# Performance work log

Measured on AMD Instinct MI355X. Metric: run time of the kernel, lower is better.

## Reference

```python
import jax, jax.numpy as jnp
import numpy as np

D_MODEL = 1024
N_HEADS = 16
D_K = D_MODEL // N_HEADS
D_FF = 4096
B, S = 4, 2048
EPS = 1e-5


def setup_inputs() -> dict:
    key = jax.random.key(0)
    ks = jax.random.split(key, 16)
    s = 0.02
    inp = {
        'x': jax.random.normal(ks[0], (B, S, D_MODEL), dtype=jnp.float32),
        'Wq': jax.random.normal(ks[1], (D_MODEL, D_MODEL), dtype=jnp.float32) * s,
        'bq': jnp.zeros((D_MODEL,), jnp.float32),
        'Wk': jax.random.normal(ks[2], (D_MODEL, D_MODEL), dtype=jnp.float32) * s,
        'bk': jnp.zeros((D_MODEL,), jnp.float32),
        'Wv': jax.random.normal(ks[3], (D_MODEL, D_MODEL), dtype=jnp.float32) * s,
        'bv': jnp.zeros((D_MODEL,), jnp.float32),
        'Wo': jax.random.normal(ks[4], (D_MODEL, D_MODEL), dtype=jnp.float32) * s,
        'bo': jnp.zeros((D_MODEL,), jnp.float32),
        'W1': jax.random.normal(ks[5], (D_MODEL, D_FF), dtype=jnp.float32) * s,
        'b1': jnp.zeros((D_FF,), jnp.float32),
        'W2': jax.random.normal(ks[6], (D_FF, D_MODEL), dtype=jnp.float32) * s,
        'b2': jnp.zeros((D_MODEL,), jnp.float32),
        'g1': jnp.ones((D_MODEL,), jnp.float32),
        'be1': jnp.zeros((D_MODEL,), jnp.float32),
        'g2': jnp.ones((D_MODEL,), jnp.float32),
        'be2': jnp.zeros((D_MODEL,), jnp.float32),
    }
    return inp


def _layernorm(x, g, b):
    mu = jnp.mean(x, axis=-1, keepdims=True)
    var = jnp.var(x, axis=-1, keepdims=True)
    return (x - mu) * jax.lax.rsqrt(var + EPS) * g + b


def reference(x, Wq, bq, Wk, bk, Wv, bv, Wo, bo, W1, b1, W2, b2, g1, be1, g2, be2):
    # Multi-head self-attention (mask=None, dropout in eval -> identity)
    q = (x @ Wq + bq).reshape(B, S, N_HEADS, D_K).transpose(0, 2, 1, 3)  # [B,H,S,Dk]
    k = (x @ Wk + bk).reshape(B, S, N_HEADS, D_K).transpose(0, 2, 1, 3)
    v = (x @ Wv + bv).reshape(B, S, N_HEADS, D_K).transpose(0, 2, 1, 3)
    scores = jnp.einsum('bhqd,bhkd->bhqk', q, k) / jnp.sqrt(jnp.float32(D_K))
    attn = jax.nn.softmax(scores, axis=-1)
    out = jnp.einsum('bhqk,bhkd->bhqd', attn, v)          # [B,H,S,Dk]
    out = out.transpose(0, 2, 1, 3).reshape(B, S, D_MODEL)
    att_out = out @ Wo + bo
    x2 = _layernorm(x + att_out, g1, be1)
    ff = jax.nn.relu(x2 @ W1 + b1) @ W2 + b2
    return _layernorm(x2 + ff, g2, be2)
```

## Files before the change

kernel.cpp:

```cpp
#include <hip/hip_runtime.h>
#include <hip/hip_bf16.h>

typedef __attribute__((ext_vector_type(8)))  __bf16 bf16x8;
typedef __attribute__((ext_vector_type(4)))  float  f32x4;
typedef __attribute__((ext_vector_type(16))) float  f32x16;

static __device__ __forceinline__ unsigned short f2bf(float x) {
    unsigned int u = __float_as_uint(x);
    unsigned int r = (u + 0x7FFFu + ((u >> 16) & 1u)) >> 16;
    return (unsigned short)r;
}
static __device__ __forceinline__ float bf2f(unsigned short u) {
    return __uint_as_float(((unsigned int)u) << 16);
}

static __device__ __forceinline__ float fast_exp2(float x) {
    float r;
    asm volatile("v_exp_f32 %0, %1\n\ts_nop 1" : "=v"(r) : "v"(x));
    return r;
}
static __device__ __forceinline__ unsigned int cvt_pk_bf16(float a, float b) {
    unsigned int r;
    asm("v_cvt_pk_bf16_f32 %0, %1, %2" : "=v"(r) : "v"(a), "v"(b));
    return r;
}

static __device__ __forceinline__ void gload_lds16(const ushort* g, ushort* l) {
    __builtin_amdgcn_global_load_lds((const __attribute__((address_space(1))) void*)g,
                                     (__attribute__((address_space(3))) void*)l, 16, 0, 0);
}

static __device__ __forceinline__ void barrier_fence() {
    __builtin_amdgcn_s_barrier();
    __builtin_amdgcn_sched_barrier(0);
    asm volatile("" ::: "memory");
}

static __device__ __forceinline__ int xcd_swz(int id, int nwg) {
    return (id & 7) * (nwg >> 3) + (id >> 3);
}

__global__ __launch_bounds__(256) void cast_bf16_kernel(const float* __restrict__ in,
                                                        ushort* __restrict__ out, int n4) {
    int i = blockIdx.x * 256 + threadIdx.x;
    if (i < n4) {
        float4 v = reinterpret_cast<const float4*>(in)[i];
        ushort4 o;
        o.x = f2bf(v.x); o.y = f2bf(v.y); o.z = f2bf(v.z); o.w = f2bf(v.w);
        reinterpret_cast<ushort4*>(out)[i] = o;
    }
}

__global__ __launch_bounds__(256) void transpose_cast_kernel(const float* __restrict__ in,
                                                             ushort* __restrict__ out,
                                                             int K, int N) {
    __shared__ float tile[32][33];
    const int tx = threadIdx.x;
    const int ty = threadIdx.y;
    const int n0 = blockIdx.x * 32;
    const int k0 = blockIdx.y * 32;
    for (int i = ty; i < 32; i += 8)
        tile[i][tx] = in[(size_t)(k0 + i) * N + n0 + tx];
    __syncthreads();
    for (int i = ty; i < 32; i += 8)
        out[(size_t)(n0 + i) * K + k0 + tx] = f2bf(tile[tx][i]);
}

__global__ __launch_bounds__(256) void transpose_cast3_kernel(const float* __restrict__ w0,
                                                              const float* __restrict__ w1,
                                                              const float* __restrict__ w2,
                                                              ushort* __restrict__ out) {
    __shared__ float tile[32][33];
    const int tx = threadIdx.x;
    const int ty = threadIdx.y;
    const int n0 = blockIdx.x * 32;
    const int k0 = blockIdx.y * 32;
    const int z  = blockIdx.z;
    const float* in = (z == 0) ? w0 : (z == 1 ? w1 : w2);
    ushort* o = out + (size_t)z * 1024 * 1024;
    for (int i = ty; i < 32; i += 8)
        tile[i][tx] = in[(size_t)(k0 + i) * 1024 + n0 + tx];
    __syncthreads();
    for (int i = ty; i < 32; i += 8)
        o[(size_t)(n0 + i) * 1024 + k0 + tx] = f2bf(tile[tx][i]);
}

template<int RELU, int OUTBF, int QKV>
__global__ __launch_bounds__(256) void gemm_p3(const ushort* __restrict__ A,
                                               const ushort* __restrict__ Bt,
                                               const float* __restrict__ b0,
                                               const float* __restrict__ b1_,
                                               const float* __restrict__ b2_,
                                               void* __restrict__ Cp,
                                               int M, int N, int K) {
    __shared__ ushort As[3][4096];
    __shared__ ushort Bs[3][4096];
    const int tid  = threadIdx.x;
    const int lane = tid & 63;
    const int w    = tid >> 6;
    const int wr   = w >> 1, wc = w & 1;
    const int nwg = gridDim.x * gridDim.y;
    int wid = xcd_swz(blockIdx.y * gridDim.x + blockIdx.x, nwg);
    const int bx = wid % gridDim.x;
    const int by = wid / gridDim.x;
    const int m0 = by * 128;
    const int n0 = bx * 128;
    const int lr = lane & 15;
    const int lk = (lane >> 4) * 8;

    const int r0 = w * 32 + (lane >> 2);
    const int c8 = (lane & 3) * 8;
    const ushort* gA0 = A  + (size_t)(m0 + r0)      * K + c8;
    const ushort* gA1 = A  + (size_t)(m0 + r0 + 16) * K + c8;
    const ushort* gB0 = Bt + (size_t)(n0 + r0)      * K + c8;
    const ushort* gB1 = Bt + (size_t)(n0 + r0 + 16) * K + c8;
    const int wb = w * 1024;

    f32x4 acc[4][4];
    const f32x4 z = {0.f, 0.f, 0.f, 0.f};
#pragma unroll
    for (int i = 0; i < 4; i++)
#pragma unroll
        for (int j = 0; j < 4; j++) acc[i][j] = z;

    const int nt = K >> 5;

#pragma unroll
    for (int t = 0; t < 2; ++t) {
        const int kn = t * 32;
        gload_lds16(gA0 + kn, &As[t][wb]);
        gload_lds16(gA1 + kn, &As[t][wb + 512]);
        gload_lds16(gB0 + kn, &Bs[t][wb]);
        gload_lds16(gB1 + kn, &Bs[t][wb + 512]);
    }

    int cur = 0;
    for (int t = 0; t < nt; ++t) {
        if (t + 1 < nt) asm volatile("s_waitcnt vmcnt(4)" ::: "memory");
        else            asm volatile("s_waitcnt vmcnt(0)" ::: "memory");
        barrier_fence();

        if (t + 2 < nt) {
            const int bi = (cur + 2 >= 3) ? cur - 1 : cur + 2;
            const int kn = (t + 2) * 32;
            gload_lds16(gA0 + kn, &As[bi][wb]);
            gload_lds16(gA1 + kn, &As[bi][wb + 512]);
            gload_lds16(gB0 + kn, &Bs[bi][wb]);
            gload_lds16(gB1 + kn, &Bs[bi][wb + 512]);
        }

        const ushort* Asb = As[cur];
        const ushort* Bsb = Bs[cur];
        bf16x8 af[4], bfr[4];
#pragma unroll
        for (int i = 0; i < 4; i++)
            af[i] = *reinterpret_cast<const bf16x8*>(&Asb[(wr * 64 + i * 16 + lr) * 32 + lk]);
#pragma unroll
        for (int j = 0; j < 4; j++)
            bfr[j] = *reinterpret_cast<const bf16x8*>(&Bsb[(wc * 64 + j * 16 + lr) * 32 + lk]);
#pragma unroll
        for (int i = 0; i < 4; i++)
#pragma unroll
            for (int j = 0; j < 4; j++)
                acc[i][j] = __builtin_amdgcn_mfma_f32_16x16x32_bf16(af[i], bfr[j], acc[i][j], 0, 0, 0);

        cur = (cur == 2) ? 0 : cur + 1;
    }

    const float* bias;
    float qscale = 1.0f;
    if (QKV) {
        bias = (n0 < 1024) ? b0 : (n0 < 2048 ? b1_ : b2_);
        if (n0 < 1024) qscale = 0.18033688f;
    } else {
        bias = b0;
    }
    const int nb = QKV ? (n0 & 1023) : n0;
    const int rbase = (lane >> 4) * 4;
#pragma unroll
    for (int i = 0; i < 4; i++) {
#pragma unroll
        for (int j = 0; j < 4; j++) {
            const int cloc = wc * 64 + j * 16 + lr;
            const float bv = bias[nb + cloc];
#pragma unroll
            for (int r = 0; r < 4; r++) {
                const int row = m0 + wr * 64 + i * 16 + rbase + r;
                float v = acc[i][j][r] + bv;
                if (RELU) v = v > 0.f ? v : 0.f;
                if (QKV)  v *= qscale;
                if (OUTBF) ((ushort*)Cp)[(size_t)row * N + n0 + cloc] = f2bf(v);
                else       ((float*)Cp)[(size_t)row * N + n0 + cloc] = v;
            }
        }
    }
}

#define ASWZ(row, col) ((row) * 64 + ((col) ^ ((((row) ^ ((row) >> 3)) & 7) << 3)))

__global__ __launch_bounds__(256, 3) void attn_kernel(const ushort* __restrict__ QKV,
                                                      ushort* __restrict__ O) {
    __shared__ ushort Ks[2][4096];
    __shared__ ushort Vt[2][4096];
    const int tid  = threadIdx.x;
    const int lane = tid & 63;
    const int w    = tid >> 6;
    const int l31  = lane & 31;
    const int hi   = lane >> 5;

    int blk = xcd_swz(blockIdx.x, gridDim.x);
    const int qb = blk & 15;
    const int h  = (blk >> 4) & 15;
    const int b  = blk >> 8;
    const int s0 = qb * 128 + w * 32;
    const size_t rowb   = (size_t)b * 2048;
    const size_t base_q = rowb * 3072 + (size_t)h * 64;
    const size_t base_k = base_q + 1024;
    const size_t base_v = base_q + 2048;
    const size_t base_o = rowb * 1024 + (size_t)h * 64;

    bf16x8 qf[4];
#pragma unroll
    for (int ks = 0; ks < 4; ks++)
        qf[ks] = *reinterpret_cast<const bf16x8*>(
            &QKV[base_q + (size_t)(s0 + l31) * 3072 + ks * 16 + 8 * hi]);

    int off8[2][4];
#pragma unroll
    for (int sub = 0; sub < 2; sub++)
#pragma unroll
        for (int ks = 0; ks < 4; ks++)
            off8[sub][ks] = ASWZ(sub * 32 + l31, ks * 16 + 8 * hi);

    const int tS  = tid >> 3;
    const int ccS = tid & 7;
    int vwoff[2][8];
#pragma unroll
    for (int i = 0; i < 2; i++)
#pragma unroll
        for (int jj = 0; jj < 8; jj++)
            vwoff[i][jj] = ASWZ(ccS * 8 + jj, tS + i * 32);
    const int t1  = tS + 32;
    const int sz0 = (tS ^ (tS >> 3)) & 7;
    const int sz1 = (t1 ^ (t1 >> 3)) & 7;
    const ushort* pK0 = QKV + base_k + (size_t)tS * 3072 + (ccS ^ sz0) * 8;
    const ushort* pK1 = QKV + base_k + (size_t)t1 * 3072 + (ccS ^ sz1) * 8;
    const ushort* pV0 = QKV + base_v + (size_t)tS * 3072 + ccS * 8;
    const ushort* pV1 = QKV + base_v + (size_t)t1 * 3072 + ccS * 8;
    const size_t step = (size_t)64 * 3072;

    gload_lds16(pK0, &Ks[0][w * 512]);
    gload_lds16(pK1, &Ks[0][2048 + w * 512]);
    {
        int4 v0 = *reinterpret_cast<const int4*>(pV0);
        int4 v1 = *reinterpret_cast<const int4*>(pV1);
        const ushort* vs0 = reinterpret_cast<const ushort*>(&v0);
        const ushort* vs1 = reinterpret_cast<const ushort*>(&v1);
#pragma unroll
        for (int jj = 0; jj < 8; jj++) Vt[0][vwoff[0][jj]] = vs0[jj];
#pragma unroll
        for (int jj = 0; jj < 8; jj++) Vt[0][vwoff[1][jj]] = vs1[jj];
    }
    pK0 += step; pK1 += step; pV0 += step; pV1 += step;
    __syncthreads();

    f32x16 oacc0, oacc1;
    for (int i = 0; i < 16; i++) { oacc0[i] = 0.f; oacc1[i] = 0.f; }
    float lacc = 0.f;
    int cur = 0;

    for (int it = 0; it < 32; ++it) {
        int4 nv0, nv1;
        if (it < 31) {
            gload_lds16(pK0, &Ks[cur ^ 1][w * 512]);
            gload_lds16(pK1, &Ks[cur ^ 1][2048 + w * 512]);
            nv0 = *reinterpret_cast<const int4*>(pV0);
            nv1 = *reinterpret_cast<const int4*>(pV1);
            pK0 += step; pK1 += step; pV0 += step; pV1 += step;
        }

        f32x16 sa0, sa1;
        for (int i = 0; i < 16; i++) { sa0[i] = 0.f; sa1[i] = 0.f; }
        __builtin_amdgcn_s_setprio(1);
#pragma unroll
        for (int ks = 0; ks < 4; ks++) {
            bf16x8 k0 = *reinterpret_cast<const bf16x8*>(&Ks[cur][off8[0][ks]]);
            sa0 = __builtin_amdgcn_mfma_f32_32x32x16_bf16(k0, qf[ks], sa0, 0, 0, 0);
        }
#pragma unroll
        for (int ks = 0; ks < 4; ks++) {
            bf16x8 k1 = *reinterpret_cast<const bf16x8*>(&Ks[cur][off8[1][ks]]);
            sa1 = __builtin_amdgcn_mfma_f32_32x32x16_bf16(k1, qf[ks], sa1, 0, 0, 0);
        }
        __builtin_amdgcn_s_setprio(0);

        unsigned pk0[8], pk1[8];
#pragma unroll
        for (int i = 0; i < 8; i++) {
            float plo = fast_exp2(sa0[2 * i]);
            float phi = fast_exp2(sa0[2 * i + 1]);
            lacc += plo + phi;
            pk0[i] = cvt_pk_bf16(plo, phi);
        }
#pragma unroll
        for (int i = 0; i < 8; i++) {
            float plo = fast_exp2(sa1[2 * i]);
            float phi = fast_exp2(sa1[2 * i + 1]);
            lacc += plo + phi;
            pk1[i] = cvt_pk_bf16(plo, phi);
        }

        __builtin_amdgcn_s_setprio(1);
#pragma unroll
        for (int ks = 0; ks < 4; ks++) {
            const int bi = 4 * (ks & 1);
            unsigned a, bb, c, d;
            if (ks < 2) { a = pk0[bi]; bb = pk0[bi + 1]; c = pk0[bi + 2]; d = pk0[bi + 3]; }
            else        { a = pk1[bi]; bb = pk1[bi + 1]; c = pk1[bi + 2]; d = pk1[bi + 3]; }
            asm("v_permlane32_swap_b32 %0, %1" : "+v"(a), "+v"(c));
            asm("v_permlane32_swap_b32 %0, %1" : "+v"(bb), "+v"(d));
            union { unsigned u[4]; bf16x8 v; } fr;
            fr.u[0] = a; fr.u[1] = bb; fr.u[2] = c; fr.u[3] = d;
            bf16x8 v0 = *reinterpret_cast<const bf16x8*>(&Vt[cur][off8[0][ks]]);
            oacc0 = __builtin_amdgcn_mfma_f32_32x32x16_bf16(fr.v, v0, oacc0, 0, 0, 0);
            bf16x8 v1 = *reinterpret_cast<const bf16x8*>(&Vt[cur][off8[1][ks]]);
            oacc1 = __builtin_amdgcn_mfma_f32_32x32x16_bf16(fr.v, v1, oacc1, 0, 0, 0);
        }
        __builtin_amdgcn_s_setprio(0);

        if (it < 31) {
            const ushort* vs0 = reinterpret_cast<const ushort*>(&nv0);
            const ushort* vs1 = reinterpret_cast<const ushort*>(&nv1);
#pragma unroll
            for (int jj = 0; jj < 8; jj++) Vt[cur ^ 1][vwoff[0][jj]] = vs0[jj];
#pragma unroll
            for (int jj = 0; jj < 8; jj++) Vt[cur ^ 1][vwoff[1][jj]] = vs1[jj];
        }
        __syncthreads();
        cur ^= 1;
    }

    const float ltot = lacc + __shfl_xor(lacc, 32);
    const float inv  = 1.f / ltot;
#pragma unroll
    for (int r = 0; r < 16; r++) {
        const int qloc = (r & 3) + 8 * (r >> 2) + 4 * hi;
        const float invq = __shfl(inv, qloc);
        const size_t rowoff = base_o + (size_t)(s0 + qloc) * 1024 + l31;
        O[rowoff]      = f2bf(oacc0[r] * invq);
        O[rowoff + 32] = f2bf(oacc1[r] * invq);
    }
}

__global__ __launch_bounds__(256) void ln_res_fb(const float* __restrict__ x,
                                                 const ushort* __restrict__ y,
                                                 const float* __restrict__ g,
                                                 const float* __restrict__ be,
                                                 ushort* __restrict__ outb) {
    const int row = blockIdx.x;
    const int tid = threadIdx.x;
    const float4 xv = reinterpret_cast<const float4*>(x + (size_t)row * 1024)[tid];
    const ushort4 yv = reinterpret_cast<const ushort4*>(y + (size_t)row * 1024)[tid];
    float v[4] = {xv.x + bf2f(yv.x), xv.y + bf2f(yv.y), xv.z + bf2f(yv.z), xv.w + bf2f(yv.w)};
    float s  = v[0] + v[1] + v[2] + v[3];
    float s2 = v[0]*v[0] + v[1]*v[1] + v[2]*v[2] + v[3]*v[3];
    for (int off = 32; off; off >>= 1) { s += __shfl_down(s, off); s2 += __shfl_down(s2, off); }
    __shared__ float red[8];
    const int w = tid >> 6, lane = tid & 63;
    if (lane == 0) { red[w] = s; red[4 + w] = s2; }
    __syncthreads();
    if (tid == 0) {
        const float ts  = red[0] + red[1] + red[2] + red[3];
        const float ts2 = red[4] + red[5] + red[6] + red[7];
        const float mu  = ts * (1.f / 1024.f);
        const float var = ts2 * (1.f / 1024.f) - mu * mu;
        red[0] = mu;
        red[1] = rsqrtf(var + 1e-5f);
    }
    __syncthreads();
    const float mu = red[0], rs = red[1];
    const float4 gv = reinterpret_cast<const float4*>(g)[tid];
    const float4 bv = reinterpret_cast<const float4*>(be)[tid];
    ushort4 ob;
    ob.x = f2bf((v[0] - mu) * rs * gv.x + bv.x);
    ob.y = f2bf((v[1] - mu) * rs * gv.y + bv.y);
    ob.z = f2bf((v[2] - mu) * rs * gv.z + bv.z);
    ob.w = f2bf((v[3] - mu) * rs * gv.w + bv.w);
    reinterpret_cast<ushort4*>(outb + (size_t)row * 1024)[tid] = ob;
}

__global__ __launch_bounds__(256) void ln_res_bb(const ushort* __restrict__ x,
                                                 const ushort* __restrict__ y,
                                                 const float* __restrict__ g,
                                                 const float* __restrict__ be,
                                                 float* __restrict__ outf) {
    const int row = blockIdx.x;
    const int tid = threadIdx.x;
    const ushort4 xv = reinterpret_cast<const ushort4*>(x + (size_t)row * 1024)[tid];
    const ushort4 yv = reinterpret_cast<const ushort4*>(y + (size_t)row * 1024)[tid];
    float v[4] = {bf2f(xv.x) + bf2f(yv.x), bf2f(xv.y) + bf2f(yv.y),
                  bf2f(xv.z) + bf2f(yv.z), bf2f(xv.w) + bf2f(yv.w)};
    float s  = v[0] + v[1] + v[2] + v[3];
    float s2 = v[0]*v[0] + v[1]*v[1] + v[2]*v[2] + v[3]*v[3];
    for (int off = 32; off; off >>= 1) { s += __shfl_down(s, off); s2 += __shfl_down(s2, off); }
    __shared__ float red[8];
    const int w = tid >> 6, lane = tid & 63;
    if (lane == 0) { red[w] = s; red[4 + w] = s2; }
    __syncthreads();
    if (tid == 0) {
        const float ts  = red[0] + red[1] + red[2] + red[3];
        const float ts2 = red[4] + red[5] + red[6] + red[7];
        const float mu  = ts * (1.f / 1024.f);
        const float var = ts2 * (1.f / 1024.f) - mu * mu;
        red[0] = mu;
        red[1] = rsqrtf(var + 1e-5f);
    }
    __syncthreads();
    const float mu = red[0], rs = red[1];
    const float4 gv = reinterpret_cast<const float4*>(g)[tid];
    const float4 bv = reinterpret_cast<const float4*>(be)[tid];
    float4 of;
    of.x = (v[0] - mu) * rs * gv.x + bv.x;
    of.y = (v[1] - mu) * rs * gv.y + bv.y;
    of.z = (v[2] - mu) * rs * gv.z + bv.z;
    of.w = (v[3] - mu) * rs * gv.w + bv.w;
    reinterpret_cast<float4*>(outf + (size_t)row * 1024)[tid] = of;
}

extern "C" void kernel_launch(void* const* d_in, const int* in_sizes, int n_in,
                              void* d_out, int out_size, void* d_ws, size_t ws_size,
                              hipStream_t stream) {
    const float* x  = (const float*)d_in[0];
    const float* Wq = (const float*)d_in[1];  const float* bq = (const float*)d_in[2];
    const float* Wk = (const float*)d_in[3];  const float* bk = (const float*)d_in[4];
    const float* Wv = (const float*)d_in[5];  const float* bv = (const float*)d_in[6];
    const float* Wo = (const float*)d_in[7];  const float* bo = (const float*)d_in[8];
    const float* W1 = (const float*)d_in[9];  const float* b1 = (const float*)d_in[10];
    const float* W2 = (const float*)d_in[11]; const float* b2 = (const float*)d_in[12];
    const float* g1 = (const float*)d_in[13]; const float* be1 = (const float*)d_in[14];
    const float* g2 = (const float*)d_in[15]; const float* be2 = (const float*)d_in[16];

    char* ws = (char*)d_ws;
    const size_t MBy = (size_t)1 << 20;
    ushort* xb    = (ushort*)(ws + 0 * MBy);
    ushort* wqkvT = (ushort*)(ws + 16 * MBy);
    ushort* woT   = (ushort*)(ws + 22 * MBy);
    ushort* w1T   = (ushort*)(ws + 24 * MBy);
    ushort* w2T   = (ushort*)(ws + 32 * MBy);
    ushort* QKVb  = (ushort*)(ws + 40 * MBy);
    ushort* AOb   = (ushort*)(ws + 88 * MBy);
    ushort* h1    = (ushort*)(ws + 40 * MBy);
    ushort* y1b   = (ushort*)(ws + 104 * MBy);
    ushort* y2b   = (ushort*)(ws + 104 * MBy);
    ushort* x2b   = (ushort*)(ws + 120 * MBy);
    (void)ws_size; (void)n_in; (void)in_sizes; (void)out_size;

    const int M = 8192;

    cast_bf16_kernel<<<(M * 1024 / 4 + 255) / 256, 256, 0, stream>>>(x, xb, M * 1024 / 4);
    dim3 tb(32, 8);
    transpose_cast3_kernel<<<dim3(32, 32, 3), tb, 0, stream>>>(Wq, Wk, Wv, wqkvT);
    transpose_cast_kernel<<<dim3(32, 32),  tb, 0, stream>>>(Wo, woT, 1024, 1024);
    transpose_cast_kernel<<<dim3(128, 32), tb, 0, stream>>>(W1, w1T, 1024, 4096);
    transpose_cast_kernel<<<dim3(32, 128), tb, 0, stream>>>(W2, w2T, 4096, 1024);

    gemm_p3<0, 1, 1><<<dim3(24, 64), 256, 0, stream>>>(xb, wqkvT, bq, bk, bv, QKVb,
                                                       M, 3072, 1024);

    attn_kernel<<<1024, 256, 0, stream>>>(QKVb, AOb);

    gemm_p3<0, 1, 0><<<dim3(8, 64), 256, 0, stream>>>(AOb, woT, bo, nullptr, nullptr, y1b,
                                                      M, 1024, 1024);

    ln_res_fb<<<M, 256, 0, stream>>>(x, y1b, g1, be1, x2b);

    gemm_p3<1, 1, 0><<<dim3(32, 64), 256, 0, stream>>>(x2b, w1T, b1, nullptr, nullptr, h1,
                                                       M, 4096, 1024);
    gemm_p3<0, 1, 0><<<dim3(8, 64), 256, 0, stream>>>(h1, w2T, b2, nullptr, nullptr, y2b,
                                                      M, 1024, 4096);

    ln_res_bb<<<M, 256, 0, stream>>>(x2b, y2b, g2, be2, (float*)d_out);
}
```

Baseline: 428.7 us.

## Enlarge GEMM tiles to 256x128 with 8 waves, BK=64 and swizzled LDS

Replaces the 128x128, 4-wave GEMM with a 256x128 tile computed by 8 waves. The K step doubles to 64 and the LDS layout uses an XOR swizzle to avoid bank conflicts on the fragment reads, and MFMA blocks are wrapped in s_setprio. The aim is better operand reuse per byte loaded, fewer barriers per unit of K, and fewer LDS conflicts. The cost is much higher LDS use (~144KB across 3 stages), which may limit occupancy, plus fewer workgroups for the N=1024 GEMMs.

```diff
diff --git a/kernel.cpp b/kernel.cpp
--- a/kernel.cpp
+++ b/kernel.cpp
@@ -86,35 +86,62 @@
 }
 
 template<int RELU, int OUTBF, int QKV>
-__global__ __launch_bounds__(256) void gemm_p3(const ushort* __restrict__ A,
-                                               const ushort* __restrict__ Bt,
-                                               const float* __restrict__ b0,
-                                               const float* __restrict__ b1_,
-                                               const float* __restrict__ b2_,
-                                               void* __restrict__ Cp,
-                                               int M, int N, int K) {
-    __shared__ ushort As[3][4096];
-    __shared__ ushort Bs[3][4096];
+__global__ __launch_bounds__(512, 2) void gemm_8p(const ushort* __restrict__ A,
+                                                  const ushort* __restrict__ Bt,
+                                                  const float* __restrict__ b0,
+                                                  const float* __restrict__ b1_,
+                                                  const float* __restrict__ b2_,
+                                                  void* __restrict__ Cp,
+                                                  int M, int N, int K) {
+    __shared__ ushort As[3][16384];
+    __shared__ ushort Bs[3][8192];
     const int tid  = threadIdx.x;
     const int lane = tid & 63;
     const int w    = tid >> 6;
-    const int wr   = w >> 1, wc = w & 1;
-    const int nwg = gridDim.x * gridDim.y;
+    const int wr   = w >> 1;
+    const int wc   = w & 1;
+    const int nwg  = gridDim.x * gridDim.y;
     int wid = xcd_swz(blockIdx.y * gridDim.x + blockIdx.x, nwg);
     const int bx = wid % gridDim.x;
     const int by = wid / gridDim.x;
-    const int m0 = by * 128;
+    const int m0 = by * 256;
     const int n0 = bx * 128;
     const int lr = lane & 15;
-    const int lk = (lane >> 4) * 8;
-
-    const int r0 = w * 32 + (lane >> 2);
-    const int c8 = (lane & 3) * 8;
-    const ushort* gA0 = A  + (size_t)(m0 + r0)      * K + c8;
-    const ushort* gA1 = A  + (size_t)(m0 + r0 + 16) * K + c8;
-    const ushort* gB0 = Bt + (size_t)(n0 + r0)      * K + c8;
-    const ushort* gB1 = Bt + (size_t)(n0 + r0 + 16) * K + c8;
-    const int wb = w * 1024;
+    const int lg = lane >> 4;
+
+    int offA[4][2], offB[4][2];
+#pragma unroll
+    for (int i = 0; i < 4; i++) {
+        const int row = wr * 64 + i * 16 + lr;
+#pragma unroll
+        for (int ks = 0; ks < 2; ks++)
+            offA[i][ks] = row * 64 + (((ks * 4 + lg) ^ (row & 7)) << 3);
+    }
+#pragma unroll
+    for (int j = 0; j < 4; j++) {
+        const int row = wc * 64 + j * 16 + lr;
+#pragma unroll
+        for (int ks = 0; ks < 2; ks++)
+            offB[j][ks] = row * 64 + (((ks * 4 + lg) ^ (row & 7)) << 3);
+    }
+
+    const int cp = lane & 7;
+    const ushort* gA[4];
+    int ldsA[4];
+#pragma unroll
+    for (int a = 0; a < 4; a++) {
+        const int row = a * 64 + w * 8 + (lane >> 3);
+        gA[a]  = A + (size_t)(m0 + row) * K + ((cp ^ (row & 7)) << 3);
+        ldsA[a] = (a * 512 + w * 64) * 8;
+    }
+    const ushort* gB[2];
+    int ldsB[2];
+#pragma unroll
+    for (int b = 0; b < 2; b++) {
+        const int row = b * 64 + w * 8 + (lane >> 3);
+        gB[b]  = Bt + (size_t)(n0 + row) * K + ((cp ^ (row & 7)) << 3);
+        ldsB[b] = (b * 512 + w * 64) * 8;
+    }
 
     f32x4 acc[4][4];
     const f32x4 z = {0.f, 0.f, 0.f, 0.f};
@@ -123,46 +150,67 @@
 #pragma unroll
         for (int j = 0; j < 4; j++) acc[i][j] = z;
 
-    const int nt = K >> 5;
+    const int nt = K >> 6;
 
 #pragma unroll
     for (int t = 0; t < 2; ++t) {
-        const int kn = t * 32;
-        gload_lds16(gA0 + kn, &As[t][wb]);
-        gload_lds16(gA1 + kn, &As[t][wb + 512]);
-        gload_lds16(gB0 + kn, &Bs[t][wb]);
-        gload_lds16(gB1 + kn, &Bs[t][wb + 512]);
+        const int kn = t * 64;
+#pragma unroll
+        for (int a = 0; a < 4; a++) gload_lds16(gA[a] + kn, &As[t][ldsA[a]]);
+#pragma unroll
+        for (int b = 0; b < 2; b++) gload_lds16(gB[b] + kn, &Bs[t][ldsB[b]]);
     }
 
     int cur = 0;
     for (int t = 0; t < nt; ++t) {
-        if (t + 1 < nt) asm volatile("s_waitcnt vmcnt(4)" ::: "memory");
+        if (t + 1 < nt) asm volatile("s_waitcnt vmcnt(6)" ::: "memory");
         else            asm volatile("s_waitcnt vmcnt(0)" ::: "memory");
         barrier_fence();
 
         if (t + 2 < nt) {
-            const int bi = (cur + 2 >= 3) ? cur - 1 : cur + 2;
-            const int kn = (t + 2) * 32;
-            gload_lds16(gA0 + kn, &As[bi][wb]);
-            gload_lds16(gA1 + kn, &As[bi][wb + 512]);
-            gload_lds16(gB0 + kn, &Bs[bi][wb]);
-            gload_lds16(gB1 + kn, &Bs[bi][wb + 512]);
+            const int bi = (cur + 2 > 2) ? cur - 1 : cur + 2;
+            const int kn = (t + 2) * 64;
+#pragma unroll
+            for (int a = 0; a < 4; a++) gload_lds16(gA[a] + kn, &As[bi][ldsA[a]]);
+#pragma unroll
+            for (int b = 0; b < 2; b++) gload_lds16(gB[b] + kn, &Bs[bi][ldsB[b]]);
         }
 
         const ushort* Asb = As[cur];
         const ushort* Bsb = Bs[cur];
-        bf16x8 af[4], bfr[4];
-#pragma unroll
-        for (int i = 0; i < 4; i++)
-            af[i] = *reinterpret_cast<const bf16x8*>(&Asb[(wr * 64 + i * 16 + lr) * 32 + lk]);
-#pragma unroll
-        for (int j = 0; j < 4; j++)
-            bfr[j] = *reinterpret_cast<const bf16x8*>(&Bsb[(wc * 64 + j * 16 + lr) * 32 + lk]);
-#pragma unroll
-        for (int i = 0; i < 4; i++)
+
+        {
+            bf16x8 af[4], bfr[4];
+#pragma unroll
+            for (int i = 0; i < 4; i++)
+                af[i] = *reinterpret_cast<const bf16x8*>(&Asb[offA[i][0]]);
 #pragma unroll
             for (int j = 0; j < 4; j++)
-                acc[i][j] = __builtin_amdgcn_mfma_f32_16x16x32_bf16(af[i], bfr[j], acc[i][j], 0, 0, 0);
+                bfr[j] = *reinterpret_cast<const bf16x8*>(&Bsb[offB[j][0]]);
+            __builtin_amdgcn_s_setprio(1);
+#pragma unroll
+            for (int i = 0; i < 4; i++)
+#pragma unroll
+                for (int j = 0; j < 4; j++)
+                    acc[i][j] = __builtin_amdgcn_mfma_f32_16x16x32_bf16(af[i], bfr[j], acc[i][j], 0, 0, 0);
+            __builtin_amdgcn_s_setprio(0);
+        }
+        {
+            bf16x8 af[4], bfr[4];
+#pragma unroll
+            for (int i = 0; i < 4; i++)
+                af[i] = *reinterpret_cast<const bf16x8*>(&Asb[offA[i][1]]);
+#pragma unroll
+            for (int j = 0; j < 4; j++)
+                bfr[j] = *reinterpret_cast<const bf16x8*>(&Bsb[offB[j][1]]);
+            __builtin_amdgcn_s_setprio(1);
+#pragma unroll
+            for (int i = 0; i < 4; i++)
+#pragma unroll
+                for (int j = 0; j < 4; j++)
+                    acc[i][j] = __builtin_amdgcn_mfma_f32_16x16x32_bf16(af[i], bfr[j], acc[i][j], 0, 0, 0);
+            __builtin_amdgcn_s_setprio(0);
+        }
 
         cur = (cur == 2) ? 0 : cur + 1;
     }
@@ -464,19 +512,19 @@
     transpose_cast_kernel<<<dim3(128, 32), tb, 0, stream>>>(W1, w1T, 1024, 4096);
     transpose_cast_kernel<<<dim3(32, 128), tb, 0, stream>>>(W2, w2T, 4096, 1024);
 
-    gemm_p3<0, 1, 1><<<dim3(24, 64), 256, 0, stream>>>(xb, wqkvT, bq, bk, bv, QKVb,
+    gemm_8p<0, 1, 1><<<dim3(24, 32), 512, 0, stream>>>(xb, wqkvT, bq, bk, bv, QKVb,
                                                        M, 3072, 1024);
 
     attn_kernel<<<1024, 256, 0, stream>>>(QKVb, AOb);
 
-    gemm_p3<0, 1, 0><<<dim3(8, 64), 256, 0, stream>>>(AOb, woT, bo, nullptr, nullptr, y1b,
+    gemm_8p<0, 1, 0><<<dim3(8, 32), 512, 0, stream>>>(AOb, woT, bo, nullptr, nullptr, y1b,
                                                       M, 1024, 1024);
 
     ln_res_fb<<<M, 256, 0, stream>>>(x, y1b, g1, be1, x2b);
 
-    gemm_p3<1, 1, 0><<<dim3(32, 64), 256, 0, stream>>>(x2b, w1T, b1, nullptr, nullptr, h1,
+    gemm_8p<1, 1, 0><<<dim3(32, 32), 512, 0, stream>>>(x2b, w1T, b1, nullptr, nullptr, h1,
                                                        M, 4096, 1024);
-    gemm_p3<0, 1, 0><<<dim3(8, 64), 256, 0, stream>>>(h1, w2T, b2, nullptr, nullptr, y2b,
+    gemm_8p<0, 1, 0><<<dim3(8, 32), 512, 0, stream>>>(h1, w2T, b2, nullptr, nullptr, y2b,
                                                       M, 1024, 4096);
 
     ln_res_bb<<<M, 256, 0, stream>>>(x2b, y2b, g2, be2, (float*)d_out);
```

Result: slower. 446.4 us (+4.1%).

## Fuse residual adds into GEMM epilogues and pack V-transpose LDS writes

Applied to the files above, without the earlier changes.

Moves the residual addition (x after the Wo projection, x2 after W2) into the GEMM epilogues, so the layernorm kernels read one bf16 tensor instead of two. The attention kernel now assigns each thread two adjacent V rows and writes pairs of bf16 values as 32-bit LDS stores, halving the scalar LDS writes during the V transpose. The exp asm loses its volatile qualifier and trailing s_nop so the compiler can schedule it. The residual is now rounded to bf16 together with the GEMM output before layernorm, which slightly changes precision.

```diff
diff --git a/kernel.cpp b/kernel.cpp
--- a/kernel.cpp
+++ b/kernel.cpp
@@ -16,7 +16,7 @@
 
 static __device__ __forceinline__ float fast_exp2(float x) {
     float r;
-    asm volatile("v_exp_f32 %0, %1\n\ts_nop 1" : "=v"(r) : "v"(x));
+    asm("v_exp_f32 %0, %1" : "=v"(r) : "v"(x));
     return r;
 }
 static __device__ __forceinline__ unsigned int cvt_pk_bf16(float a, float b) {
@@ -85,12 +85,13 @@
         o[(size_t)(n0 + i) * 1024 + k0 + tx] = f2bf(tile[tx][i]);
 }
 
-template<int RELU, int OUTBF, int QKV>
+template<int RELU, int OUTBF, int QKV, int RES>
 __global__ __launch_bounds__(256) void gemm_p3(const ushort* __restrict__ A,
                                                const ushort* __restrict__ Bt,
                                                const float* __restrict__ b0,
                                                const float* __restrict__ b1_,
                                                const float* __restrict__ b2_,
+                                               const void* __restrict__ xres,
                                                void* __restrict__ Cp,
                                                int M, int N, int K) {
     __shared__ ushort As[3][4096];
@@ -187,6 +188,8 @@
             for (int r = 0; r < 4; r++) {
                 const int row = m0 + wr * 64 + i * 16 + rbase + r;
                 float v = acc[i][j][r] + bv;
+                if (RES == 1) v += ((const float*)xres)[(size_t)row * N + n0 + cloc];
+                if (RES == 2) v += bf2f(((const ushort*)xres)[(size_t)row * N + n0 + cloc]);
                 if (RELU) v = v > 0.f ? v : 0.f;
                 if (QKV)  v *= qscale;
                 if (OUTBF) ((ushort*)Cp)[(size_t)row * N + n0 + cloc] = f2bf(v);
@@ -232,21 +235,19 @@
         for (int ks = 0; ks < 4; ks++)
             off8[sub][ks] = ASWZ(sub * 32 + l31, ks * 16 + 8 * hi);
 
-    const int tS  = tid >> 3;
+    const int tS2 = tid >> 3;
     const int ccS = tid & 7;
-    int vwoff[2][8];
-#pragma unroll
-    for (int i = 0; i < 2; i++)
-#pragma unroll
-        for (int jj = 0; jj < 8; jj++)
-            vwoff[i][jj] = ASWZ(ccS * 8 + jj, tS + i * 32);
-    const int t1  = tS + 32;
-    const int sz0 = (tS ^ (tS >> 3)) & 7;
-    const int sz1 = (t1 ^ (t1 >> 3)) & 7;
-    const ushort* pK0 = QKV + base_k + (size_t)tS * 3072 + (ccS ^ sz0) * 8;
-    const ushort* pK1 = QKV + base_k + (size_t)t1 * 3072 + (ccS ^ sz1) * 8;
-    const ushort* pV0 = QKV + base_v + (size_t)tS * 3072 + ccS * 8;
-    const ushort* pV1 = QKV + base_v + (size_t)t1 * 3072 + ccS * 8;
+    int voff[8];
+#pragma unroll
+    for (int jj = 0; jj < 8; jj++)
+        voff[jj] = ASWZ(ccS * 8 + jj, 2 * tS2);
+    const int tk1 = tS2 + 32;
+    const int sz0 = (tS2 ^ (tS2 >> 3)) & 7;
+    const int sz1 = (tk1 ^ (tk1 >> 3)) & 7;
+    const ushort* pK0 = QKV + base_k + (size_t)tS2 * 3072 + (ccS ^ sz0) * 8;
+    const ushort* pK1 = QKV + base_k + (size_t)tk1 * 3072 + (ccS ^ sz1) * 8;
+    const ushort* pV0 = QKV + base_v + (size_t)(2 * tS2)     * 3072 + ccS * 8;
+    const ushort* pV1 = QKV + base_v + (size_t)(2 * tS2 + 1) * 3072 + ccS * 8;
     const size_t step = (size_t)64 * 3072;
 
     gload_lds16(pK0, &Ks[0][w * 512]);
@@ -257,9 +258,9 @@
         const ushort* vs0 = reinterpret_cast<const ushort*>(&v0);
         const ushort* vs1 = reinterpret_cast<const ushort*>(&v1);
 #pragma unroll
-        for (int jj = 0; jj < 8; jj++) Vt[0][vwoff[0][jj]] = vs0[jj];
-#pragma unroll
-        for (int jj = 0; jj < 8; jj++) Vt[0][vwoff[1][jj]] = vs1[jj];
+        for (int jj = 0; jj < 8; jj++)
+            *reinterpret_cast<unsigned*>(&Vt[0][voff[jj]]) =
+                (unsigned)vs0[jj] | ((unsigned)vs1[jj] << 16);
     }
     pK0 += step; pK1 += step; pV0 += step; pV1 += step;
     __syncthreads();
@@ -332,9 +333,9 @@
             const ushort* vs0 = reinterpret_cast<const ushort*>(&nv0);
             const ushort* vs1 = reinterpret_cast<const ushort*>(&nv1);
 #pragma unroll
-            for (int jj = 0; jj < 8; jj++) Vt[cur ^ 1][vwoff[0][jj]] = vs0[jj];
-#pragma unroll
-            for (int jj = 0; jj < 8; jj++) Vt[cur ^ 1][vwoff[1][jj]] = vs1[jj];
+            for (int jj = 0; jj < 8; jj++)
+                *reinterpret_cast<unsigned*>(&Vt[cur ^ 1][voff[jj]]) =
+                    (unsigned)vs0[jj] | ((unsigned)vs1[jj] << 16);
         }
         __syncthreads();
         cur ^= 1;
@@ -352,16 +353,15 @@
     }
 }
 
-__global__ __launch_bounds__(256) void ln_res_fb(const float* __restrict__ x,
-                                                 const ushort* __restrict__ y,
-                                                 const float* __restrict__ g,
-                                                 const float* __restrict__ be,
-                                                 ushort* __restrict__ outb) {
+template<int OUTBF>
+__global__ __launch_bounds__(256) void ln_one(const ushort* __restrict__ zin,
+                                              const float* __restrict__ g,
+                                              const float* __restrict__ be,
+                                              void* __restrict__ out) {
     const int row = blockIdx.x;
     const int tid = threadIdx.x;
-    const float4 xv = reinterpret_cast<const float4*>(x + (size_t)row * 1024)[tid];
-    const ushort4 yv = reinterpret_cast<const ushort4*>(y + (size_t)row * 1024)[tid];
-    float v[4] = {xv.x + bf2f(yv.x), xv.y + bf2f(yv.y), xv.z + bf2f(yv.z), xv.w + bf2f(yv.w)};
+    const ushort4 zv = reinterpret_cast<const ushort4*>(zin + (size_t)row * 1024)[tid];
+    float v[4] = {bf2f(zv.x), bf2f(zv.y), bf2f(zv.z), bf2f(zv.w)};
     float s  = v[0] + v[1] + v[2] + v[3];
     float s2 = v[0]*v[0] + v[1]*v[1] + v[2]*v[2] + v[3]*v[3];
     for (int off = 32; off; off >>= 1) { s += __shfl_down(s, off); s2 += __shfl_down(s2, off); }
@@ -381,50 +381,19 @@
     const float mu = red[0], rs = red[1];
     const float4 gv = reinterpret_cast<const float4*>(g)[tid];
     const float4 bv = reinterpret_cast<const float4*>(be)[tid];
-    ushort4 ob;
-    ob.x = f2bf((v[0] - mu) * rs * gv.x + bv.x);
-    ob.y = f2bf((v[1] - mu) * rs * gv.y + bv.y);
-    ob.z = f2bf((v[2] - mu) * rs * gv.z + bv.z);
-    ob.w = f2bf((v[3] - mu) * rs * gv.w + bv.w);
-    reinterpret_cast<ushort4*>(outb + (size_t)row * 1024)[tid] = ob;
-}
-
-__global__ __launch_bounds__(256) void ln_res_bb(const ushort* __restrict__ x,
-                                                 const ushort* __restrict__ y,
-                                                 const float* __restrict__ g,
-                                                 const float* __restrict__ be,
-                                                 float* __restrict__ outf) {
-    const int row = blockIdx.x;
-    const int tid = threadIdx.x;
-    const ushort4 xv = reinterpret_cast<const ushort4*>(x + (size_t)row * 1024)[tid];
-    const ushort4 yv = reinterpret_cast<const ushort4*>(y + (size_t)row * 1024)[tid];
-    float v[4] = {bf2f(xv.x) + bf2f(yv.x), bf2f(xv.y) + bf2f(yv.y),
-                  bf2f(xv.z) + bf2f(yv.z), bf2f(xv.w) + bf2f(yv.w)};
-    float s  = v[0] + v[1] + v[2] + v[3];
-    float s2 = v[0]*v[0] + v[1]*v[1] + v[2]*v[2] + v[3]*v[3];
-    for (int off = 32; off; off >>= 1) { s += __shfl_down(s, off); s2 += __shfl_down(s2, off); }
-    __shared__ float red[8];
-    const int w = tid >> 6, lane = tid & 63;
-    if (lane == 0) { red[w] = s; red[4 + w] = s2; }
-    __syncthreads();
-    if (tid == 0) {
-        const float ts  = red[0] + red[1] + red[2] + red[3];
-        const float ts2 = red[4] + red[5] + red[6] + red[7];
-        const float mu  = ts * (1.f / 1024.f);
-        const float var = ts2 * (1.f / 1024.f) - mu * mu;
-        red[0] = mu;
-        red[1] = rsqrtf(var + 1e-5f);
-    }
-    __syncthreads();
-    const float mu = red[0], rs = red[1];
-    const float4 gv = reinterpret_cast<const float4*>(g)[tid];
-    const float4 bv = reinterpret_cast<const float4*>(be)[tid];
-    float4 of;
-    of.x = (v[0] - mu) * rs * gv.x + bv.x;
-    of.y = (v[1] - mu) * rs * gv.y + bv.y;
-    of.z = (v[2] - mu) * rs * gv.z + bv.z;
-    of.w = (v[3] - mu) * rs * gv.w + bv.w;
-    reinterpret_cast<float4*>(outf + (size_t)row * 1024)[tid] = of;
+    float o0 = (v[0] - mu) * rs * gv.x + bv.x;
+    float o1 = (v[1] - mu) * rs * gv.y + bv.y;
+    float o2 = (v[2] - mu) * rs * gv.z + bv.z;
+    float o3 = (v[3] - mu) * rs * gv.w + bv.w;
+    if (OUTBF) {
+        ushort4 ob;
+        ob.x = f2bf(o0); ob.y = f2bf(o1); ob.z = f2bf(o2); ob.w = f2bf(o3);
+        reinterpret_cast<ushort4*>((ushort*)out + (size_t)row * 1024)[tid] = ob;
+    } else {
+        float4 of;
+        of.x = o0; of.y = o1; of.z = o2; of.w = o3;
+        reinterpret_cast<float4*>((float*)out + (size_t)row * 1024)[tid] = of;
+    }
 }
 
 extern "C" void kernel_launch(void* const* d_in, const int* in_sizes, int n_in,
@@ -450,8 +419,8 @@
     ushort* QKVb  = (ushort*)(ws + 40 * MBy);
     ushort* AOb   = (ushort*)(ws + 88 * MBy);
     ushort* h1    = (ushort*)(ws + 40 * MBy);
-    ushort* y1b   = (ushort*)(ws + 104 * MBy);
-    ushort* y2b   = (ushort*)(ws + 104 * MBy);
+    ushort* z1b   = (ushort*)(ws + 104 * MBy);
+    ushort* z2b   = (ushort*)(ws + 104 * MBy);
     ushort* x2b   = (ushort*)(ws + 120 * MBy);
     (void)ws_size; (void)n_in; (void)in_sizes; (void)out_size;
 
@@ -464,20 +433,20 @@
     transpose_cast_kernel<<<dim3(128, 32), tb, 0, stream>>>(W1, w1T, 1024, 4096);
     transpose_cast_kernel<<<dim3(32, 128), tb, 0, stream>>>(W2, w2T, 4096, 1024);
 
-    gemm_p3<0, 1, 1><<<dim3(24, 64), 256, 0, stream>>>(xb, wqkvT, bq, bk, bv, QKVb,
-                                                       M, 3072, 1024);
+    gemm_p3<0, 1, 1, 0><<<dim3(24, 64), 256, 0, stream>>>(xb, wqkvT, bq, bk, bv, nullptr,
+                                                          QKVb, M, 3072, 1024);
 
     attn_kernel<<<1024, 256, 0, stream>>>(QKVb, AOb);
 
-    gemm_p3<0, 1, 0><<<dim3(8, 64), 256, 0, stream>>>(AOb, woT, bo, nullptr, nullptr, y1b,
-                                                      M, 1024, 1024);
-
-    ln_res_fb<<<M, 256, 0, stream>>>(x, y1b, g1, be1, x2b);
-
-    gemm_p3<1, 1, 0><<<dim3(32, 64), 256, 0, stream>>>(x2b, w1T, b1, nullptr, nullptr, h1,
-                                                       M, 4096, 1024);
-    gemm_p3<0, 1, 0><<<dim3(8, 64), 256, 0, stream>>>(h1, w2T, b2, nullptr, nullptr, y2b,
-                                                      M, 1024, 4096);
-
-    ln_res_bb<<<M, 256, 0, stream>>>(x2b, y2b, g2, be2, (float*)d_out);
-}
+    gemm_p3<0, 1, 0, 1><<<dim3(8, 64), 256, 0, stream>>>(AOb, woT, bo, nullptr, nullptr, x,
+                                                         z1b, M, 1024, 1024);
+
+    ln_one<1><<<M, 256, 0, stream>>>(z1b, g1, be1, x2b);
+
+    gemm_p3<1, 1, 0, 0><<<dim3(32, 64), 256, 0, stream>>>(x2b, w1T, b1, nullptr, nullptr,
+                                                          nullptr, h1, M, 4096, 1024);
+    gemm_p3<0, 1, 0, 2><<<dim3(8, 64), 256, 0, stream>>>(h1, w2T, b2, nullptr, nullptr, x2b,
+                                                         z2b, M, 1024, 4096);
+
+    ln_one<0><<<M, 256, 0, stream>>>(z2b, g2, be2, (float*)d_out);
+}
```

Measured after the change: 408.1 us. 4.8% less time.
